# Optimization experiments

Measured on AMD Instinct MI355X. Metric: run time of the kernel, lower is better.

Reference implementation:

```python
import jax, jax.numpy as jnp
import numpy as np

B, S = 1, 2048            # one prefill sequence, flattened to n_tokens = B*S
HID = 4096
NH, NKV, HD = 32, 8, 128  # query heads, kv heads, head dim
G, M = NKV, NH // NKV     # kv groups, query heads per group
THETA = 1e6


def setup_inputs() -> dict:
    key = jax.random.key(0)
    ks = jax.random.split(key, 5)
    h = jax.random.normal(ks[0], (B * S, HID), dtype=jnp.float32)
    position_ids = jnp.tile(jnp.arange(S, dtype=jnp.int32), B)
    wq = jax.random.normal(ks[1], (NH * HD, HID), dtype=jnp.float32) * 0.02
    wk = jax.random.normal(ks[2], (NKV * HD, HID), dtype=jnp.float32) * 0.02
    wv = jax.random.normal(ks[3], (NKV * HD, HID), dtype=jnp.float32) * 0.02
    wo = jax.random.normal(ks[4], (HID, NH * HD), dtype=jnp.float32) * 0.02
    return {"h": h, "position_ids": position_ids, "wq": wq, "wk": wk, "wv": wv, "wo": wo}


def _rope_cos_sin(position_ids):
    # non-interleaved (half-split) RoPE, default inv_freq with theta=1e6
    inv_freq = 1.0 / (THETA ** (jnp.arange(0, HD, 2, dtype=jnp.float32) / HD))  # [HD/2]
    freqs = position_ids.astype(jnp.float32)[:, None] * inv_freq[None, :]       # [n, HD/2]
    return jnp.cos(freqs)[:, None, :], jnp.sin(freqs)[:, None, :]               # broadcast over heads


def _apply_rope(x, cos, sin):
    x1, x2 = jnp.split(x, 2, axis=-1)
    return jnp.concatenate([x1 * cos - x2 * sin, x2 * cos + x1 * sin], axis=-1)


def reference(h, position_ids, wq, wk, wv, wo):
    n = h.shape[0]
    q = (h @ wq.T).reshape(n, NH, HD)
    k = (h @ wk.T).reshape(n, NKV, HD)
    v = (h @ wv.T).reshape(B, S, NKV, HD)

    cos, sin = _rope_cos_sin(position_ids)
    q = _apply_rope(q, cos, sin).reshape(B, S, G, M, HD)
    k = _apply_rope(k, cos, sin).reshape(B, S, G, HD)

    scale = 1.0 / np.sqrt(HD).astype(np.float32)
    # grouped-query attention: each kv head g serves M query heads
    scores = jnp.einsum('bqgmd,bkgd->bgmqk', q, k) * scale      # [B,G,M,S,S]
    causal = jnp.tril(jnp.ones((S, S), dtype=bool))
    scores = jnp.where(causal, scores, jnp.finfo(scores.dtype).min)
    p = jax.nn.softmax(scores, axis=-1)
    o = jnp.einsum('bgmqk,bkgd->bqgmd', p, v).reshape(n, NH * HD)
    return o @ wo.T
```

## Files before the change

kernel.cpp:

```cpp
#include <hip/hip_runtime.h>
#include <hip/hip_bf16.h>

#define S_LEN 2048
#define HID 4096
#define NH 32
#define NKV 8
#define HD 128
#define NQKV 6144

typedef unsigned short u16;
typedef unsigned int u32;
typedef __bf16 bf16x8 __attribute__((ext_vector_type(8)));
typedef float f32x4 __attribute__((ext_vector_type(4)));

__device__ __forceinline__ float bf2f(u16 u) {
    union { u32 i; float f; } x; x.i = ((u32)u) << 16; return x.f;
}
__device__ __forceinline__ u16 f2bf(float f) {
    union { float f; u32 i; } x; x.f = f;
    u32 r = x.i + 0x7fffu + ((x.i >> 16) & 1u);
    return (u16)(r >> 16);
}
__device__ __forceinline__ u32 pack2(float a, float b) {
    return (u32)f2bf(a) | ((u32)f2bf(b) << 16);
}
__device__ __forceinline__ void gld16(const u16* g, u16* l) {
    __builtin_amdgcn_global_load_lds(
        (const __attribute__((address_space(1))) u32*)g,
        (__attribute__((address_space(3))) u32*)l, 16, 0, 0);
}

__global__ __launch_bounds__(256) void cvt_f32_bf16(
    const float* __restrict__ src, u16* __restrict__ dst, int n8)
{
    int i = blockIdx.x * 256 + threadIdx.x;
    if (i >= n8) return;
    const float4* s = (const float4*)src + (size_t)i * 2;
    float4 x0 = s[0], x1 = s[1];
    uint4 p;
    p.x = pack2(x0.x, x0.y); p.y = pack2(x0.z, x0.w);
    p.z = pack2(x1.x, x1.y); p.w = pack2(x1.z, x1.w);
    *((uint4*)dst + i) = p;
}

template <bool OUTBF16>
__global__ __launch_bounds__(256) void gemm128(
    const u16* __restrict__ X, const u16* __restrict__ W,
    void* __restrict__ C, int K, int ldc)
{
    __shared__ __align__(16) u16 As[128 * 32];
    __shared__ __align__(16) u16 Bs[128 * 32];

    const int tid  = threadIdx.x;
    const int w    = tid >> 6;
    const int lane = tid & 63;
    const int quad = lane >> 4;
    const int n16  = lane & 15;

    int id = blockIdx.y * gridDim.x + blockIdx.x;
    const int nwg = gridDim.x * gridDim.y;
    if ((nwg & 7) == 0) {
        const int cpx = nwg >> 3;
        id = (id & 7) * cpx + (id >> 3);
    }
    const int m0 = (id / gridDim.x) * 128;
    const int n0 = (id % gridDim.x) * 128;

    const int wr   = (w >> 1) * 64;
    const int wc   = (w & 1) * 64;

    const int c0 = tid;
    const int c1 = tid + 256;

    f32x4 acc[4][4] = {};

    for (int k0 = 0; k0 < K; k0 += 32) {
        __syncthreads();
        gld16(X + (size_t)(m0 + (c0 >> 2)) * K + k0 + (c0 & 3) * 8,
              As + (size_t)(w * 64) * 8);
        gld16(X + (size_t)(m0 + (c1 >> 2)) * K + k0 + (c1 & 3) * 8,
              As + (size_t)(256 + w * 64) * 8);
        gld16(W + (size_t)(n0 + (c0 >> 2)) * K + k0 + (c0 & 3) * 8,
              Bs + (size_t)(w * 64) * 8);
        gld16(W + (size_t)(n0 + (c1 >> 2)) * K + k0 + (c1 & 3) * 8,
              Bs + (size_t)(256 + w * 64) * 8);
        __syncthreads();

        bf16x8 a[4], b[4];
#pragma unroll
        for (int t = 0; t < 4; ++t) {
            a[t] = *reinterpret_cast<const bf16x8*>(As + (wr + t * 16 + n16) * 32 + quad * 8);
            b[t] = *reinterpret_cast<const bf16x8*>(Bs + (wc + t * 16 + n16) * 32 + quad * 8);
        }
#pragma unroll
        for (int mt = 0; mt < 4; ++mt)
#pragma unroll
            for (int nt = 0; nt < 4; ++nt)
                acc[mt][nt] = __builtin_amdgcn_mfma_f32_16x16x32_bf16(
                    a[mt], b[nt], acc[mt][nt], 0, 0, 0);
    }

#pragma unroll
    for (int mt = 0; mt < 4; ++mt) {
        const int row0 = m0 + wr + mt * 16 + quad * 4;
#pragma unroll
        for (int nt = 0; nt < 4; ++nt) {
            const int col = n0 + wc + nt * 16 + n16;
#pragma unroll
            for (int r = 0; r < 4; ++r) {
                if constexpr (OUTBF16)
                    ((u16*)C)[(size_t)(row0 + r) * ldc + col] = f2bf(acc[mt][nt][r]);
                else
                    ((float*)C)[(size_t)(row0 + r) * ldc + col] = acc[mt][nt][r];
            }
        }
    }
}

template <bool XF32, bool OUTBF16>
__global__ __launch_bounds__(256) void gemm_bt(
    const void* __restrict__ Xv,
    const float* __restrict__ W0, int r1,
    const float* __restrict__ W1, int r2,
    const float* __restrict__ W2,
    void* __restrict__ C, int K, int ldc)
{
    __shared__ u16 Xs[64][48];
    __shared__ u16 Ws[64][48];

    const int tid  = threadIdx.x;
    const int w    = tid >> 6;
    const int lane = tid & 63;
    const int m0   = blockIdx.y * 64;
    const int n0   = blockIdx.x * 64;

    const int sr = tid >> 2;
    const int sc = (tid & 3) * 8;

    const float* xrow32 = nullptr;
    const u16*   xrow16 = nullptr;
    if constexpr (XF32) xrow32 = (const float*)Xv + (size_t)(m0 + sr) * K;
    else                xrow16 = (const u16*)Xv + (size_t)(m0 + sr) * K;

    const int wr = n0 + sr;
    const float* wrow;
    if (wr < r1)      wrow = W0 + (size_t)wr * K;
    else if (wr < r2) wrow = W1 + (size_t)(wr - r1) * K;
    else              wrow = W2 + (size_t)(wr - r2) * K;

    f32x4 acc[4] = {};
    const int mrow = w * 16 + (lane & 15);
    const int nrow = lane & 15;
    const int kq   = (lane >> 4) * 8;

    for (int k0 = 0; k0 < K; k0 += 32) {
        __syncthreads();
        if constexpr (XF32) {
            float4 x0 = *reinterpret_cast<const float4*>(xrow32 + k0 + sc);
            float4 x1 = *reinterpret_cast<const float4*>(xrow32 + k0 + sc + 4);
            uint4 p;
            p.x = pack2(x0.x, x0.y); p.y = pack2(x0.z, x0.w);
            p.z = pack2(x1.x, x1.y); p.w = pack2(x1.z, x1.w);
            *reinterpret_cast<uint4*>(&Xs[sr][sc]) = p;
        } else {
            *reinterpret_cast<uint4*>(&Xs[sr][sc]) =
                *reinterpret_cast<const uint4*>(xrow16 + k0 + sc);
        }
        {
            float4 w0v = *reinterpret_cast<const float4*>(wrow + k0 + sc);
            float4 w1v = *reinterpret_cast<const float4*>(wrow + k0 + sc + 4);
            uint4 p;
            p.x = pack2(w0v.x, w0v.y); p.y = pack2(w0v.z, w0v.w);
            p.z = pack2(w1v.x, w1v.y); p.w = pack2(w1v.z, w1v.w);
            *reinterpret_cast<uint4*>(&Ws[sr][sc]) = p;
        }
        __syncthreads();
        bf16x8 a = *reinterpret_cast<const bf16x8*>(&Xs[mrow][kq]);
#pragma unroll
        for (int t = 0; t < 4; ++t) {
            bf16x8 b = *reinterpret_cast<const bf16x8*>(&Ws[t * 16 + nrow][kq]);
            acc[t] = __builtin_amdgcn_mfma_f32_16x16x32_bf16(a, b, acc[t], 0, 0, 0);
        }
    }

    const int mb = m0 + w * 16 + ((lane >> 4) << 2);
#pragma unroll
    for (int t = 0; t < 4; ++t) {
        const int col = n0 + t * 16 + (lane & 15);
#pragma unroll
        for (int i = 0; i < 4; ++i) {
            if constexpr (OUTBF16)
                ((u16*)C)[(size_t)(mb + i) * ldc + col] = f2bf(acc[t][i]);
            else
                ((float*)C)[(size_t)(mb + i) * ldc + col] = acc[t][i];
        }
    }
}

__global__ __launch_bounds__(256) void rope_kernel(
    const u16* __restrict__ qkv, const int* __restrict__ pos,
    u16* __restrict__ qb, u16* __restrict__ kb, u16* __restrict__ vb)
{
    const int n   = blockIdx.x;
    const int tid = threadIdx.x;
    const float scale = 0.08838834764831845f;
    __shared__ float cs[64], sn[64];
    if (tid < 64) {
        float p   = (float)pos[n];
        float inv = powf(1.0e6f, -(float)tid / 64.0f);
        float f   = p * inv;
        cs[tid] = cosf(f);
        sn[tid] = sinf(f);
    }
    __syncthreads();
    const u16* row = qkv + (size_t)n * NQKV;

    for (int i = tid; i < NH * 64; i += 256) {
        int h = i >> 6, j = i & 63;
        float x1 = bf2f(row[h * HD + j]), x2 = bf2f(row[h * HD + j + 64]);
        size_t base = ((size_t)h * S_LEN + n) * HD;
        qb[base + j]      = f2bf((x1 * cs[j] - x2 * sn[j]) * scale);
        qb[base + j + 64] = f2bf((x2 * cs[j] + x1 * sn[j]) * scale);
    }
    for (int i = tid; i < NKV * 64; i += 256) {
        int g = i >> 6, j = i & 63;
        const u16* kr = row + NH * HD + g * HD;
        float x1 = bf2f(kr[j]), x2 = bf2f(kr[j + 64]);
        size_t base = ((size_t)g * S_LEN + n) * HD;
        kb[base + j]      = f2bf(x1 * cs[j] - x2 * sn[j]);
        kb[base + j + 64] = f2bf(x2 * cs[j] + x1 * sn[j]);
    }
    for (int i = tid; i < NKV * HD; i += 256) {
        int g = i >> 7, d = i & 127;
        vb[((size_t)g * S_LEN + n) * HD + d] = row[NH * HD + NKV * HD + g * HD + d];
    }
}

__global__ __launch_bounds__(512, 2) void attn_mfma(
    const u16* __restrict__ qb, const u16* __restrict__ kb,
    const u16* __restrict__ vb, u16* __restrict__ ao)
{
    __shared__ __align__(16) u16 smem[32768];

    const int tid  = threadIdx.x;
    const int gtid = tid & 255;
    const int grp  = tid >> 8;
    const int wg   = (tid >> 6) & 3;
    const int lane = tid & 63;
    const int quad = lane >> 4;
    const int n16  = lane & 15;
    const int h    = blockIdx.y;
    const int g    = h >> 2;
    const int NQT  = S_LEN / 64;

    u16* KPg = smem + grp * 8192;
    u16* Vtg = smem + 16384 + grp * 8192;
    float* mrg = reinterpret_cast<float*>(smem);

    const u16* kbase = kb + (size_t)g * S_LEN * HD;
    const u16* vbase = vb + (size_t)g * S_LEN * HD;
    const int xsw = (n16 & 7) << 3;

    const int krow = gtid >> 4;
    const int kcol = ((gtid & 15) ^ ((gtid >> 4) & 7)) << 3;
    u16* kdst = KPg + (size_t)(wg * 64) * 8;

    for (int half = 0; half < 2; ++half) {
        const int qt = half ? (NQT - 1 - blockIdx.x) : blockIdx.x;
        const int q0 = qt * 64;

        bf16x8 qf[4];
        {
            const u16* qrow = qb + ((size_t)h * S_LEN + q0 + wg * 16 + n16) * HD;
#pragma unroll
            for (int s = 0; s < 4; ++s)
                qf[s] = *reinterpret_cast<const bf16x8*>(qrow + s * 32 + quad * 8);
        }

        f32x4 of[8] = {};
        float mrow[4], lrow[4];
#pragma unroll
        for (int r = 0; r < 4; ++r) { mrow[r] = -1e30f; lrow[r] = 0.0f; }

        uint4 vreg[4];
        auto load_v = [&](int k0) {
#pragma unroll
            for (int i = 0; i < 4; ++i)
                vreg[i] = *reinterpret_cast<const uint4*>(
                    vbase + (size_t)(k0 + lane) * HD + wg * 8 + i * 32);
        };
        load_v(grp * 64);

        const int ntiles = qt + 1;
        const int nIt = (ntiles + 1) >> 1;
        for (int it = 0; it < nIt; ++it) {
            const int kt = 2 * it + grp;
            const bool act = (kt < ntiles);

            __syncthreads();
            if (act) {
                const int k0 = kt * 64;
#pragma unroll
                for (int i = 0; i < 4; ++i)
                    gld16(kbase + (size_t)(k0 + i * 16 + krow) * HD + kcol,
                          kdst + (size_t)(i * 256) * 8);
#pragma unroll
                for (int i = 0; i < 4; ++i) {
                    const int d0 = wg * 8 + i * 32;
                    const u32 vw[4] = {vreg[i].x, vreg[i].y, vreg[i].z, vreg[i].w};
#pragma unroll
                    for (int t = 0; t < 4; ++t) {
                        const int r0 = d0 + 2 * t;
                        Vtg[r0 * 64 + (lane ^ ((r0 & 7) << 3))]             = (u16)(vw[t] & 0xffff);
                        Vtg[(r0 + 1) * 64 + (lane ^ (((r0 + 1) & 7) << 3))] = (u16)(vw[t] >> 16);
                    }
                }
            }
            __syncthreads();
            if (kt + 2 < ntiles) load_v((kt + 2) * 64);

            f32x4 sc[4] = {};
            if (act) {
#pragma unroll
                for (int s = 0; s < 4; ++s) {
#pragma unroll
                    for (int t = 0; t < 4; ++t) {
                        bf16x8 bf = *reinterpret_cast<const bf16x8*>(
                            &KPg[(t * 16 + n16) * 128 + ((s * 32 + quad * 8) ^ xsw)]);
                        sc[t] = __builtin_amdgcn_mfma_f32_16x16x32_bf16(qf[s], bf, sc[t], 0, 0, 0);
                    }
                }
                if (kt == qt) {
                    const int qbase = q0 + wg * 16 + quad * 4;
#pragma unroll
                    for (int t = 0; t < 4; ++t) {
                        int key = kt * 64 + t * 16 + n16;
#pragma unroll
                        for (int r = 0; r < 4; ++r)
                            if (key > qbase + r) sc[t][r] = -1e30f;
                    }
                }
            }

            __syncthreads();

            if (act) {
#pragma unroll
                for (int r = 0; r < 4; ++r) {
                    float mx = fmaxf(fmaxf(sc[0][r], sc[1][r]), fmaxf(sc[2][r], sc[3][r]));
                    mx = fmaxf(mx, __shfl_xor(mx, 1));
                    mx = fmaxf(mx, __shfl_xor(mx, 2));
                    mx = fmaxf(mx, __shfl_xor(mx, 4));
                    mx = fmaxf(mx, __shfl_xor(mx, 8));
                    float mnew  = fmaxf(mrow[r], mx);
                    float alpha = __expf(mrow[r] - mnew);
                    float ls = 0.0f;
                    const int pr = quad * 4 + r;
#pragma unroll
                    for (int t = 0; t < 4; ++t) {
                        float p = __expf(sc[t][r] - mnew);
                        KPg[(wg * 16 + pr) * 64 + ((t * 16 + n16) ^ ((pr & 7) << 3))] = f2bf(p);
                        ls += p;
                    }
                    ls += __shfl_xor(ls, 1);
                    ls += __shfl_xor(ls, 2);
                    ls += __shfl_xor(ls, 4);
                    ls += __shfl_xor(ls, 8);
                    lrow[r] = lrow[r] * alpha + ls;
                    mrow[r] = mnew;
#pragma unroll
                    for (int nt = 0; nt < 8; ++nt) of[nt][r] *= alpha;
                }
                __threadfence_block();

#pragma unroll
                for (int s = 0; s < 2; ++s) {
                    bf16x8 af = *reinterpret_cast<const bf16x8*>(
                        &KPg[(wg * 16 + n16) * 64 + ((s * 32 + quad * 8) ^ xsw)]);
#pragma unroll
                    for (int nt = 0; nt < 8; ++nt) {
                        bf16x8 bf = *reinterpret_cast<const bf16x8*>(
                            &Vtg[(nt * 16 + n16) * 64 + ((s * 32 + quad * 8) ^ xsw)]);
                        of[nt] = __builtin_amdgcn_mfma_f32_16x16x32_bf16(af, bf, of[nt], 0, 0, 0);
                    }
                }
            }
        }

        __syncthreads();
        if (grp == 1) {
            float* dst = mrg + ((size_t)(wg * 64 + lane)) * 40;
#pragma unroll
            for (int nt = 0; nt < 8; ++nt)
#pragma unroll
                for (int r = 0; r < 4; ++r) dst[nt * 4 + r] = of[nt][r];
#pragma unroll
            for (int r = 0; r < 4; ++r) { dst[32 + r] = mrow[r]; dst[36 + r] = lrow[r]; }
        }
        __syncthreads();
        if (grp == 0) {
            const float* src = mrg + ((size_t)(wg * 64 + lane)) * 40;
#pragma unroll
            for (int r = 0; r < 4; ++r) {
                const float mB = src[32 + r], lB = src[36 + r];
                const float m  = fmaxf(mrow[r], mB);
                const float a  = __expf(mrow[r] - m);
                const float b  = __expf(mB - m);
                const float inv = 1.0f / (lrow[r] * a + lB * b);
                u16* dst = ao + (size_t)(q0 + wg * 16 + quad * 4 + r) * (NH * HD) + h * HD + n16;
#pragma unroll
                for (int nt = 0; nt < 8; ++nt)
                    dst[nt * 16] = f2bf((of[nt][r] * a + src[nt * 4 + r] * b) * inv);
            }
        }
        __syncthreads();
    }
}

extern "C" void kernel_launch(void* const* d_in, const int* in_sizes, int n_in,
                              void* d_out, int out_size, void* d_ws, size_t ws_size,
                              hipStream_t stream)
{
    const float* h   = (const float*)d_in[0];
    const int*   pos = (const int*)d_in[1];
    const float* wq  = (const float*)d_in[2];
    const float* wk  = (const float*)d_in[3];
    const float* wv  = (const float*)d_in[4];
    const float* wo  = (const float*)d_in[5];

    char* ws = (char*)d_ws;

    if (ws_size >= 92274688ull) {
        u16* hb     = (u16*)(ws);
        u16* wqkv_b = (u16*)(ws + 16777216);
        u16* ao     = (u16*)(ws + 16777216);
        u16* kb     = (u16*)(ws + 33554432);
        u16* vb     = (u16*)(ws + 37748736);
        u16* wo_b   = (u16*)(ws + 41943040);
        u16* qkv    = (u16*)(ws + 67108864);
        u16* qb     = hb;

        cvt_f32_bf16<<<4096, 256, 0, stream>>>(h, hb, 1048576);
        cvt_f32_bf16<<<8192, 256, 0, stream>>>(wq, wqkv_b, 2097152);
        cvt_f32_bf16<<<2048, 256, 0, stream>>>(wk, wqkv_b + 16777216, 524288);
        cvt_f32_bf16<<<2048, 256, 0, stream>>>(wv, wqkv_b + 20971520, 524288);

        gemm128<true><<<dim3(NQKV / 128, S_LEN / 128), 256, 0, stream>>>(
            hb, wqkv_b, qkv, HID, NQKV);
        rope_kernel<<<S_LEN, 256, 0, stream>>>(qkv, pos, qb, kb, vb);
        cvt_f32_bf16<<<8192, 256, 0, stream>>>(wo, wo_b, 2097152);
        attn_mfma<<<dim3(S_LEN / 128, NH), 512, 0, stream>>>(qb, kb, vb, ao);
        gemm128<false><<<dim3(HID / 128, S_LEN / 128), 256, 0, stream>>>(
            ao, wo_b, d_out, NH * HD, HID);
    } else {
        u16* qkv = (u16*)(ws);
        u16* qb  = (u16*)(ws + 25165824);
        u16* kb  = (u16*)(ws + 41943040);
        u16* vb  = (u16*)(ws + 46137344);
        u16* ao  = (u16*)(ws + 50331648);

        dim3 g1(NQKV / 64, S_LEN / 64);
        gemm_bt<true, true><<<g1, 256, 0, stream>>>(
            h, wq, NH * HD, wk, NH * HD + NKV * HD, wv, qkv, HID, NQKV);
        rope_kernel<<<S_LEN, 256, 0, stream>>>(qkv, pos, qb, kb, vb);
        attn_mfma<<<dim3(S_LEN / 128, NH), 512, 0, stream>>>(qb, kb, vb, ao);
        dim3 g2(HID / 64, S_LEN / 64);
        gemm_bt<false, false><<<g2, 256, 0, stream>>>(
            ao, wo, HID, wo, HID, wo, d_out, NH * HD, HID);
    }
}
```

Measured before the change: 568.2 us.

## Fuse RoPE and head-split into QKV GEMM epilogue; merge input conversions

The four fp32-to-bf16 conversion launches for h, wq, wk and wv become one kernel. The QKV GEMM now applies RoPE (and the query scale) in its epilogue and writes q, k and v straight into head-major buffers. To make that possible, each warp's B-tile columns are remapped so it holds both the x1 and x2 halves of a head. This removes the rope_kernel launch and the round trip of the intermediate qkv buffer through memory, at the cost of per-element sin/cos/pow in the GEMM epilogue and strided scalar stores.

```diff
diff --git a/kernel.cpp b/kernel.cpp
--- a/kernel.cpp
+++ b/kernel.cpp
@@ -43,10 +43,31 @@
     *((uint4*)dst + i) = p;
 }
 
-template <bool OUTBF16>
+__global__ __launch_bounds__(256) void cvt_all(
+    const float* __restrict__ h, const float* __restrict__ wq,
+    const float* __restrict__ wk, const float* __restrict__ wv,
+    u16* __restrict__ hb, u16* __restrict__ wqkvb)
+{
+    int i = blockIdx.x * 256 + threadIdx.x;
+    const float* src; u16* dst; int off;
+    if (i < 1048576)      { src = h;  dst = hb;               off = i; }
+    else if (i < 3145728) { src = wq; dst = wqkvb;            off = i - 1048576; }
+    else if (i < 3670016) { src = wk; dst = wqkvb + 16777216; off = i - 3145728; }
+    else                  { src = wv; dst = wqkvb + 20971520; off = i - 3670016; }
+    const float4* s = (const float4*)src + (size_t)off * 2;
+    float4 x0 = s[0], x1 = s[1];
+    uint4 p;
+    p.x = pack2(x0.x, x0.y); p.y = pack2(x0.z, x0.w);
+    p.z = pack2(x1.x, x1.y); p.w = pack2(x1.z, x1.w);
+    *((uint4*)dst + off) = p;
+}
+
+template <int EPI>
 __global__ __launch_bounds__(256) void gemm128(
     const u16* __restrict__ X, const u16* __restrict__ W,
-    void* __restrict__ C, int K, int ldc)
+    void* __restrict__ C, int K, int ldc,
+    const int* __restrict__ pos,
+    u16* __restrict__ qbO, u16* __restrict__ kbO, u16* __restrict__ vbO)
 {
     __shared__ __align__(16) u16 As[128 * 32];
     __shared__ __align__(16) u16 Bs[128 * 32];
@@ -66,8 +87,8 @@
     const int m0 = (id / gridDim.x) * 128;
     const int n0 = (id % gridDim.x) * 128;
 
-    const int wr   = (w >> 1) * 64;
-    const int wc   = (w & 1) * 64;
+    const int wr = (w >> 1) * 64;
+    const int wc = (w & 1) * 64;
 
     const int c0 = tid;
     const int c1 = tid + 256;
@@ -89,8 +110,11 @@
         bf16x8 a[4], b[4];
 #pragma unroll
         for (int t = 0; t < 4; ++t) {
+            const int bc = (EPI == 2)
+                ? ((w & 1) * 32 + (t & 1) * 16 + (t >> 1) * 64)
+                : (wc + t * 16);
             a[t] = *reinterpret_cast<const bf16x8*>(As + (wr + t * 16 + n16) * 32 + quad * 8);
-            b[t] = *reinterpret_cast<const bf16x8*>(Bs + (wc + t * 16 + n16) * 32 + quad * 8);
+            b[t] = *reinterpret_cast<const bf16x8*>(Bs + (bc + n16) * 32 + quad * 8);
         }
 #pragma unroll
         for (int mt = 0; mt < 4; ++mt)
@@ -100,6 +124,59 @@
                     a[mt], b[nt], acc[mt][nt], 0, 0, 0);
     }
 
+    if constexpr (EPI == 2) {
+        __syncthreads();
+        int* posS = (int*)As;
+        if (tid < 128) posS[tid] = pos[m0 + tid];
+        __syncthreads();
+
+        const int ht = n0 >> 7;
+        if (ht < 40) {
+            u16* out = (ht < 32) ? qbO : kbO;
+            const int hh = (ht < 32) ? ht : ht - 32;
+            const float qs = (ht < 32) ? 0.08838834764831845f : 1.0f;
+            float invj[2];
+#pragma unroll
+            for (int t = 0; t < 2; ++t) {
+                const int j = (w & 1) * 32 + t * 16 + n16;
+                invj[t] = powf(1.0e6f, -(float)j / 64.0f);
+            }
+#pragma unroll
+            for (int mt = 0; mt < 4; ++mt) {
+#pragma unroll
+                for (int r = 0; r < 4; ++r) {
+                    const int row = wr + mt * 16 + quad * 4 + r;
+                    const float p = (float)posS[row];
+                    const size_t base = ((size_t)hh * S_LEN + m0 + row) * HD;
+#pragma unroll
+                    for (int t = 0; t < 2; ++t) {
+                        const int j = (w & 1) * 32 + t * 16 + n16;
+                        const float f = p * invj[t];
+                        const float cv = cosf(f), sv = sinf(f);
+                        const float x1 = acc[mt][t][r], x2 = acc[mt][t + 2][r];
+                        out[base + j]      = f2bf((x1 * cv - x2 * sv) * qs);
+                        out[base + j + 64] = f2bf((x2 * cv + x1 * sv) * qs);
+                    }
+                }
+            }
+        } else {
+            const int gg = ht - 40;
+#pragma unroll
+            for (int mt = 0; mt < 4; ++mt)
+#pragma unroll
+                for (int nt = 0; nt < 4; ++nt) {
+                    const int d = (w & 1) * 32 + (nt & 1) * 16 + (nt >> 1) * 64 + n16;
+#pragma unroll
+                    for (int r = 0; r < 4; ++r) {
+                        const int row = wr + mt * 16 + quad * 4 + r;
+                        vbO[((size_t)gg * S_LEN + m0 + row) * HD + d] =
+                            f2bf(acc[mt][nt][r]);
+                    }
+                }
+        }
+        return;
+    }
+
 #pragma unroll
     for (int mt = 0; mt < 4; ++mt) {
         const int row0 = m0 + wr + mt * 16 + quad * 4;
@@ -108,7 +185,7 @@
             const int col = n0 + wc + nt * 16 + n16;
 #pragma unroll
             for (int r = 0; r < 4; ++r) {
-                if constexpr (OUTBF16)
+                if constexpr (EPI == 1)
                     ((u16*)C)[(size_t)(row0 + r) * ldc + col] = f2bf(acc[mt][nt][r]);
                 else
                     ((float*)C)[(size_t)(row0 + r) * ldc + col] = acc[mt][nt][r];
@@ -433,25 +510,19 @@
     if (ws_size >= 92274688ull) {
         u16* hb     = (u16*)(ws);
         u16* wqkv_b = (u16*)(ws + 16777216);
-        u16* ao     = (u16*)(ws + 16777216);
-        u16* kb     = (u16*)(ws + 33554432);
-        u16* vb     = (u16*)(ws + 37748736);
-        u16* wo_b   = (u16*)(ws + 41943040);
-        u16* qkv    = (u16*)(ws + 67108864);
-        u16* qb     = hb;
-
-        cvt_f32_bf16<<<4096, 256, 0, stream>>>(h, hb, 1048576);
-        cvt_f32_bf16<<<8192, 256, 0, stream>>>(wq, wqkv_b, 2097152);
-        cvt_f32_bf16<<<2048, 256, 0, stream>>>(wk, wqkv_b + 16777216, 524288);
-        cvt_f32_bf16<<<2048, 256, 0, stream>>>(wv, wqkv_b + 20971520, 524288);
-
-        gemm128<true><<<dim3(NQKV / 128, S_LEN / 128), 256, 0, stream>>>(
-            hb, wqkv_b, qkv, HID, NQKV);
-        rope_kernel<<<S_LEN, 256, 0, stream>>>(qkv, pos, qb, kb, vb);
+        u16* qb     = (u16*)(ws + 67108864);
+        u16* kb     = (u16*)(ws + 83886080);
+        u16* vb     = (u16*)(ws + 88080384);
+        u16* wo_b   = (u16*)(ws);
+        u16* ao     = (u16*)(ws + 33554432);
+
+        cvt_all<<<16384, 256, 0, stream>>>(h, wq, wk, wv, hb, wqkv_b);
+        gemm128<2><<<dim3(NQKV / 128, S_LEN / 128), 256, 0, stream>>>(
+            hb, wqkv_b, nullptr, HID, 0, pos, qb, kb, vb);
         cvt_f32_bf16<<<8192, 256, 0, stream>>>(wo, wo_b, 2097152);
         attn_mfma<<<dim3(S_LEN / 128, NH), 512, 0, stream>>>(qb, kb, vb, ao);
-        gemm128<false><<<dim3(HID / 128, S_LEN / 128), 256, 0, stream>>>(
-            ao, wo_b, d_out, NH * HD, HID);
+        gemm128<0><<<dim3(HID / 128, S_LEN / 128), 256, 0, stream>>>(
+            ao, wo_b, d_out, NH * HD, HID, nullptr, nullptr, nullptr, nullptr);
     } else {
         u16* qkv = (u16*)(ws);
         u16* qb  = (u16*)(ws + 25165824);
```

Result: slower. 1.907 ms (+235.5%).
